# Optimization experiments

Measured on AMD Instinct MI355X. Metric: run time of the kernel, lower is better.

The kernel has to match this reference:

```python
import jax, jax.numpy as jnp
import numpy as np

N1, N2, D = 256, 256, 1024


def setup_inputs() -> dict:
    key = jax.random.key(0)
    k1, k2, k3, k4, k5, k6, k7 = jax.random.split(key, 7)
    return {
        "features1": jax.random.normal(k1, (N1, D), dtype=jnp.float32),
        "features2": jax.random.normal(k2, (N2, D), dtype=jnp.float32),
        "mask_cross": jax.random.randint(k3, (N1, N2), 0, 2, dtype=jnp.int32),
        "mask1": jax.random.randint(k4, (N1, N1), 0, 2, dtype=jnp.int32),
        "mask2": jax.random.randint(k5, (N2, N2), 0, 2, dtype=jnp.int32),
        "mask_sents1": jax.random.randint(k6, (N1,), 0, 2, dtype=jnp.int32).astype(bool),
        "mask_sents2": jax.random.randint(k7, (N2,), 0, 2, dtype=jnp.int32).astype(bool),
    }


def _compute_loss(sim, mask, sel):
    # sim: [R, C] similarities; mask: [R, C] in {0,1}; sel: [R] row selector in {0,1}.
    # Torch code masked-selects rows (mask_sents) and pos/neg entries per row, then
    # sums -logsigmoid(sim_pos - sim_neg) over all (pos, neg) pairs. Rows with zero
    # pos or zero neg contribute 0 loss and 0 pairs, so the data-dependent branch is
    # exactly reproduced by multiplicative masking.
    mp = mask * sel[:, None]          # selected positive mask [R, C]
    mn = 1.0 - mask                   # negative mask [R, C]
    # -logsigmoid(x) == softplus(-x)
    nls = jax.nn.softplus(-(sim[:, :, None] - sim[:, None, :]))  # [R, C, C]
    loss = jnp.einsum('ij,ik,ijk->', mp, mn, nls)
    pair_num = jnp.sum(mp.sum(axis=1) * mn.sum(axis=1) * sel)
    return loss, pair_num


def reference(features1, features2, mask_cross, mask1, mask2, mask_sents1, mask_sents2):
    # sim_type == 'dot': no normalization; temperature is unused by the math.
    mc = mask_cross.astype(jnp.float32)
    m1 = mask1.astype(jnp.float32)
    m2 = mask2.astype(jnp.float32)
    s1 = mask_sents1.astype(jnp.float32)
    s2 = mask_sents2.astype(jnp.float32)

    sim12 = features1 @ features2.T   # [N1, N2]
    sim11 = features1 @ features1.T   # [N1, N1]
    sim22 = features2 @ features2.T   # [N2, N2]

    l1, p1 = _compute_loss(sim12, mc, s1)
    l2, p2 = _compute_loss(sim12.T, mc.T, s2)
    l3, p3 = _compute_loss(sim11, m1, s1)
    l4, p4 = _compute_loss(sim22, m2, s2)

    loss = l1 + l2 + l3 + l4
    pair_num = p1 + p2 + p3 + p4
    return jnp.where(pair_num > 0, loss / jnp.maximum(pair_num, 1.0), loss)
```

## Files before the change

### kernel.cpp

```cpp
#include <hip/hip_runtime.h>
#include <hip/hip_bf16.h>
#include <math.h>


#define NN 256
#define DD 1024

typedef __attribute__((ext_vector_type(8))) short short8;
typedef __attribute__((ext_vector_type(4))) float f32x4;

__device__ __forceinline__ unsigned short f32_to_bf16_rne(float x) {
    unsigned int u = __float_as_uint(x);
    u += 0x7fffu + ((u >> 16) & 1u);
    return (unsigned short)(u >> 16);
}

__global__ __launch_bounds__(256) void convert_prep_kernel(
        const float* __restrict__ f1, const float* __restrict__ f2,
        unsigned short* __restrict__ b1, unsigned short* __restrict__ b2,
        const void* ms1, const void* ms2,
        float* sel1, float* sel2,
        double* lossAcc, unsigned long long* pairAcc) {
    const int bid = blockIdx.x;
    const int tid = threadIdx.x;
    if (bid < 512) {
        const float* src = (bid < 256) ? f1 : f2;
        unsigned short* dst = (bid < 256) ? b1 : b2;
        int base = ((bid & 255) * 256 + tid) * 4;
        float4 v = *(const float4*)(src + base);
        ushort4 o;
        o.x = f32_to_bf16_rne(v.x);
        o.y = f32_to_bf16_rne(v.y);
        o.z = f32_to_bf16_rne(v.z);
        o.w = f32_to_bf16_rne(v.w);
        *(ushort4*)(dst + base) = o;
    } else {
        __shared__ int nz1, nz2;
        if (tid == 0) { nz1 = 0; nz2 = 0; }
        __syncthreads();
        const unsigned char* c1 = (const unsigned char*)ms1;
        const unsigned char* c2 = (const unsigned char*)ms2;
        if ((tid & 3) != 0) {
            if (c1[tid] != 0) atomicOr(&nz1, 1);
            if (c2[tid] != 0) atomicOr(&nz2, 1);
        }
        __syncthreads();
        sel1[tid] = (nz1 != 0) ? (c1[tid] ? 1.0f : 0.0f)
                               : (float)((const int*)ms1)[tid];
        sel2[tid] = (nz2 != 0) ? (c2[tid] ? 1.0f : 0.0f)
                               : (float)((const int*)ms2)[tid];
        if (tid == 0) { *lossAcc = 0.0; *pairAcc = 0ULL; }
    }
}

__global__ __launch_bounds__(256) void gemm_mfma(
        const unsigned short* __restrict__ b1,
        const unsigned short* __restrict__ b2,
        float* __restrict__ sims) {
    const int gwave = blockIdx.x * 4 + (threadIdx.x >> 6);
    const int m = gwave >> 8;
    const int t = gwave & 255;
    const int tr = t >> 4, tc = t & 15;
    const unsigned short* A  = (m == 2) ? b2 : b1;
    const unsigned short* Bm = (m == 0) ? b2 : ((m == 1) ? b1 : b2);
    float* C = sims + m * (NN * NN);

    const int lane = threadIdx.x & 63;
    const int r = lane & 15;
    const int quad = lane >> 4;

    const unsigned short* aptr = A  + (tr * 16 + r) * DD + quad * 8;
    const unsigned short* bptr = Bm + (tc * 16 + r) * DD + quad * 8;

    f32x4 acc = {0.f, 0.f, 0.f, 0.f};
#pragma unroll 8
    for (int k0 = 0; k0 < DD; k0 += 32) {
        short8 af = *(const short8*)(aptr + k0);
        short8 bf = *(const short8*)(bptr + k0);
        acc = __builtin_amdgcn_mfma_f32_16x16x32_bf16(af, bf, acc, 0, 0, 0);
    }
    const int row0 = tr * 16 + quad * 4;
    const int col = tc * 16 + (lane & 15);
#pragma unroll
    for (int rr = 0; rr < 4; rr++) {
        C[(row0 + rr) * NN + col] = acc[rr];
    }
}

__global__ __launch_bounds__(256) void loss_kernel(
        const float* __restrict__ sims,
        const int* __restrict__ mc,
        const int* __restrict__ m1,
        const int* __restrict__ m2,
        const float* __restrict__ sel1,
        const float* __restrict__ sel2,
        double* lossAcc, unsigned long long* pairAcc) {
    const int i = blockIdx.x;
    const int c = blockIdx.y;
    const int tid = threadIdx.x;

    const float* sim12 = sims;
    const float* sim11 = sims + NN * NN;
    const float* sim22 = sims + 2 * NN * NN;

    float sel, simv;
    int maskv;
    if (c == 0) {
        sel = sel1[i]; simv = sim12[i * NN + tid]; maskv = mc[i * NN + tid];
    } else if (c == 1) {
        sel = sel2[i]; simv = sim12[tid * NN + i]; maskv = mc[tid * NN + i];
    } else if (c == 2) {
        sel = sel1[i]; simv = sim11[i * NN + tid]; maskv = m1[i * NN + tid];
    } else {
        sel = sel2[i]; simv = sim22[i * NN + tid]; maskv = m2[i * NN + tid];
    }
    if (sel == 0.0f) return;

    const float LOG2E = 1.4426950408889634f;
    const float LN2   = 0.6931471805599453f;

    __shared__ float sPos[NN];
    __shared__ float sNeg[NN];
    __shared__ int wcnt[4];
    __shared__ float red[4];

    const int lane = tid & 63;
    const int w = tid >> 6;
    const bool pos = (maskv != 0);
    unsigned long long bal = __ballot(pos);
    if (lane == 0) wcnt[w] = __popcll(bal);
    __syncthreads();

    int posBase = 0, np_ = 0;
#pragma unroll
    for (int q = 0; q < 4; q++) {
        int v = wcnt[q];
        if (q < w) posBase += v;
        np_ += v;
    }
    const int nn_ = NN - np_;

    const unsigned long long ltmask = (1ull << lane) - 1ull;
    const int pp = __popcll(bal & ltmask);
    const float tval = simv * LOG2E;
    if (pos) sPos[posBase + pp] = tval;
    else     sNeg[(w * 64 - posBase) + (lane - pp)] = tval;
    __syncthreads();

    if (np_ == 0 || nn_ == 0) return;
    if (tid == 0) atomicAdd(pairAcc, (unsigned long long)(np_ * nn_));

    const float tn = (tid < nn_) ? sNeg[tid] : -1e30f;
    float accL = 0.f, accM = 0.f;
    for (int jj = 0; jj < np_; jj++) {
        float sp = sPos[jj];
        float x2 = tn - sp;
        float e = __builtin_amdgcn_exp2f(-fabsf(x2));
        accL += __builtin_amdgcn_logf(1.0f + e);
        accM += fmaxf(x2, 0.0f);
    }
    float local = (accL + accM) * LN2;

#pragma unroll
    for (int off = 32; off > 0; off >>= 1) local += __shfl_down(local, off, 64);
    if (lane == 0) red[w] = local;
    __syncthreads();
    if (tid == 0) {
        double bsum = (double)red[0] + (double)red[1] +
                      (double)red[2] + (double)red[3];
        atomicAdd(lossAcc, bsum);
    }
}

__global__ void finalize_kernel(const double* lossAcc,
                                const unsigned long long* pairAcc,
                                float* out) {
    double loss = *lossAcc;
    unsigned long long p = *pairAcc;
    double r = (p > 0ULL) ? (loss / (double)p) : loss;
    out[0] = (float)r;
}

extern "C" void kernel_launch(void* const* d_in, const int* in_sizes, int n_in,
                              void* d_out, int out_size, void* d_ws, size_t ws_size,
                              hipStream_t stream) {
    const float* f1 = (const float*)d_in[0];
    const float* f2 = (const float*)d_in[1];
    const int* mc = (const int*)d_in[2];
    const int* m1 = (const int*)d_in[3];
    const int* m2 = (const int*)d_in[4];
    const void* ms1 = d_in[5];
    const void* ms2 = d_in[6];

    char* ws = (char*)d_ws;
    float* sims          = (float*)ws;
    unsigned short* b1   = (unsigned short*)(ws + 786432);
    unsigned short* b2   = (unsigned short*)(ws + 1310720);
    float* sel1          = (float*)(ws + 1835008);
    float* sel2          = (float*)(ws + 1836032);
    double* lossAcc      = (double*)(ws + 1837056);
    unsigned long long* pairAcc = (unsigned long long*)(ws + 1837064);

    convert_prep_kernel<<<513, 256, 0, stream>>>(f1, f2, b1, b2, ms1, ms2,
                                                 sel1, sel2, lossAcc, pairAcc);
    gemm_mfma<<<192, 256, 0, stream>>>(b1, b2, sims);
    loss_kernel<<<dim3(256, 4), 256, 0, stream>>>(sims, mc, m1, m2, sel1, sel2,
                                                  lossAcc, pairAcc);
    finalize_kernel<<<1, 1, 0, stream>>>(lossAcc, pairAcc, (float*)d_out);
}
```

Baseline: 90.29 us.

## Fuse bf16 conversion into GEMM and finalize into loss kernel via done counter

The GEMM now reads fp32 features directly and converts them to bf16 in registers, so the separate conversion pass and its intermediate buffers are gone. The finalize step moves into the loss kernel through a last-block-done atomic counter. Together these take the pipeline from four launches to two. The cost is that the GEMM fetches twice as many bytes per MFMA and does redundant conversions, and every loss block does an extra atomic and fence.

```diff
diff --git a/kernel.cpp b/kernel.cpp
--- a/kernel.cpp
+++ b/kernel.cpp
@@ -1,5 +1,4 @@
 #include <hip/hip_runtime.h>
-#include <hip/hip_bf16.h>
 #include <math.h>
 
 
@@ -15,26 +14,16 @@
     return (unsigned short)(u >> 16);
 }
 
-__global__ __launch_bounds__(256) void convert_prep_kernel(
+__global__ __launch_bounds__(256) void gemm_prep_kernel(
         const float* __restrict__ f1, const float* __restrict__ f2,
-        unsigned short* __restrict__ b1, unsigned short* __restrict__ b2,
         const void* ms1, const void* ms2,
+        float* __restrict__ sims,
         float* sel1, float* sel2,
-        double* lossAcc, unsigned long long* pairAcc) {
+        double* lossAcc, unsigned long long* pairAcc, unsigned int* doneCnt) {
     const int bid = blockIdx.x;
     const int tid = threadIdx.x;
-    if (bid < 512) {
-        const float* src = (bid < 256) ? f1 : f2;
-        unsigned short* dst = (bid < 256) ? b1 : b2;
-        int base = ((bid & 255) * 256 + tid) * 4;
-        float4 v = *(const float4*)(src + base);
-        ushort4 o;
-        o.x = f32_to_bf16_rne(v.x);
-        o.y = f32_to_bf16_rne(v.y);
-        o.z = f32_to_bf16_rne(v.z);
-        o.w = f32_to_bf16_rne(v.w);
-        *(ushort4*)(dst + base) = o;
-    } else {
+
+    if (bid == 192) {
         __shared__ int nz1, nz2;
         if (tid == 0) { nz1 = 0; nz2 = 0; }
         __syncthreads();
@@ -49,34 +38,49 @@
                                : (float)((const int*)ms1)[tid];
         sel2[tid] = (nz2 != 0) ? (c2[tid] ? 1.0f : 0.0f)
                                : (float)((const int*)ms2)[tid];
-        if (tid == 0) { *lossAcc = 0.0; *pairAcc = 0ULL; }
-    }
-}
-
-__global__ __launch_bounds__(256) void gemm_mfma(
-        const unsigned short* __restrict__ b1,
-        const unsigned short* __restrict__ b2,
-        float* __restrict__ sims) {
-    const int gwave = blockIdx.x * 4 + (threadIdx.x >> 6);
+        if (tid == 0) { *lossAcc = 0.0; *pairAcc = 0ULL; *doneCnt = 0u; }
+        return;
+    }
+
+    const int gwave = bid * 4 + (tid >> 6);
     const int m = gwave >> 8;
     const int t = gwave & 255;
     const int tr = t >> 4, tc = t & 15;
-    const unsigned short* A  = (m == 2) ? b2 : b1;
-    const unsigned short* Bm = (m == 0) ? b2 : ((m == 1) ? b1 : b2);
+    const float* A  = (m == 2) ? f2 : f1;
+    const float* Bm = (m == 0) ? f2 : ((m == 1) ? f1 : f2);
     float* C = sims + m * (NN * NN);
 
-    const int lane = threadIdx.x & 63;
+    const int lane = tid & 63;
     const int r = lane & 15;
     const int quad = lane >> 4;
 
-    const unsigned short* aptr = A  + (tr * 16 + r) * DD + quad * 8;
-    const unsigned short* bptr = Bm + (tc * 16 + r) * DD + quad * 8;
+    const float* aptr = A  + (tr * 16 + r) * DD + quad * 8;
+    const float* bptr = Bm + (tc * 16 + r) * DD + quad * 8;
 
     f32x4 acc = {0.f, 0.f, 0.f, 0.f};
-#pragma unroll 8
+#pragma unroll 4
     for (int k0 = 0; k0 < DD; k0 += 32) {
-        short8 af = *(const short8*)(aptr + k0);
-        short8 bf = *(const short8*)(bptr + k0);
+        float4 a0 = *(const float4*)(aptr + k0);
+        float4 a1 = *(const float4*)(aptr + k0 + 4);
+        float4 b0 = *(const float4*)(bptr + k0);
+        float4 b1 = *(const float4*)(bptr + k0 + 4);
+        short8 af, bf;
+        af[0] = (short)f32_to_bf16_rne(a0.x);
+        af[1] = (short)f32_to_bf16_rne(a0.y);
+        af[2] = (short)f32_to_bf16_rne(a0.z);
+        af[3] = (short)f32_to_bf16_rne(a0.w);
+        af[4] = (short)f32_to_bf16_rne(a1.x);
+        af[5] = (short)f32_to_bf16_rne(a1.y);
+        af[6] = (short)f32_to_bf16_rne(a1.z);
+        af[7] = (short)f32_to_bf16_rne(a1.w);
+        bf[0] = (short)f32_to_bf16_rne(b0.x);
+        bf[1] = (short)f32_to_bf16_rne(b0.y);
+        bf[2] = (short)f32_to_bf16_rne(b0.z);
+        bf[3] = (short)f32_to_bf16_rne(b0.w);
+        bf[4] = (short)f32_to_bf16_rne(b1.x);
+        bf[5] = (short)f32_to_bf16_rne(b1.y);
+        bf[6] = (short)f32_to_bf16_rne(b1.z);
+        bf[7] = (short)f32_to_bf16_rne(b1.w);
         acc = __builtin_amdgcn_mfma_f32_16x16x32_bf16(af, bf, acc, 0, 0, 0);
     }
     const int row0 = tr * 16 + quad * 4;
@@ -87,14 +91,15 @@
     }
 }
 
-__global__ __launch_bounds__(256) void loss_kernel(
+__global__ __launch_bounds__(256) void loss_finalize_kernel(
         const float* __restrict__ sims,
         const int* __restrict__ mc,
         const int* __restrict__ m1,
         const int* __restrict__ m2,
         const float* __restrict__ sel1,
         const float* __restrict__ sel2,
-        double* lossAcc, unsigned long long* pairAcc) {
+        double* lossAcc, unsigned long long* pairAcc,
+        unsigned int* doneCnt, float* out) {
     const int i = blockIdx.x;
     const int c = blockIdx.y;
     const int tid = threadIdx.x;
@@ -103,82 +108,93 @@
     const float* sim11 = sims + NN * NN;
     const float* sim22 = sims + 2 * NN * NN;
 
-    float sel, simv;
-    int maskv;
-    if (c == 0) {
-        sel = sel1[i]; simv = sim12[i * NN + tid]; maskv = mc[i * NN + tid];
-    } else if (c == 1) {
-        sel = sel2[i]; simv = sim12[tid * NN + i]; maskv = mc[tid * NN + i];
-    } else if (c == 2) {
-        sel = sel1[i]; simv = sim11[i * NN + tid]; maskv = m1[i * NN + tid];
-    } else {
-        sel = sel2[i]; simv = sim22[i * NN + tid]; maskv = m2[i * NN + tid];
-    }
-    if (sel == 0.0f) return;
-
-    const float LOG2E = 1.4426950408889634f;
-    const float LN2   = 0.6931471805599453f;
-
-    __shared__ float sPos[NN];
-    __shared__ float sNeg[NN];
-    __shared__ int wcnt[4];
-    __shared__ float red[4];
-
-    const int lane = tid & 63;
-    const int w = tid >> 6;
-    const bool pos = (maskv != 0);
-    unsigned long long bal = __ballot(pos);
-    if (lane == 0) wcnt[w] = __popcll(bal);
-    __syncthreads();
-
-    int posBase = 0, np_ = 0;
+    float sel;
+    if (c == 0)      sel = sel1[i];
+    else if (c == 1) sel = sel2[i];
+    else if (c == 2) sel = sel1[i];
+    else             sel = sel2[i];
+
+    if (sel != 0.0f) {
+        float simv;
+        int maskv;
+        if (c == 0) {
+            simv = sim12[i * NN + tid]; maskv = mc[i * NN + tid];
+        } else if (c == 1) {
+            simv = sim12[tid * NN + i]; maskv = mc[tid * NN + i];
+        } else if (c == 2) {
+            simv = sim11[i * NN + tid]; maskv = m1[i * NN + tid];
+        } else {
+            simv = sim22[i * NN + tid]; maskv = m2[i * NN + tid];
+        }
+
+        const float LOG2E = 1.4426950408889634f;
+        const float LN2   = 0.6931471805599453f;
+
+        __shared__ float sPos[NN];
+        __shared__ float sNeg[NN];
+        __shared__ int wcnt[4];
+        __shared__ float red[4];
+
+        const int lane = tid & 63;
+        const int w = tid >> 6;
+        const bool pos = (maskv != 0);
+        unsigned long long bal = __ballot(pos);
+        if (lane == 0) wcnt[w] = __popcll(bal);
+        __syncthreads();
+
+        int posBase = 0, np_ = 0;
 #pragma unroll
-    for (int q = 0; q < 4; q++) {
-        int v = wcnt[q];
-        if (q < w) posBase += v;
-        np_ += v;
-    }
-    const int nn_ = NN - np_;
-
-    const unsigned long long ltmask = (1ull << lane) - 1ull;
-    const int pp = __popcll(bal & ltmask);
-    const float tval = simv * LOG2E;
-    if (pos) sPos[posBase + pp] = tval;
-    else     sNeg[(w * 64 - posBase) + (lane - pp)] = tval;
-    __syncthreads();
-
-    if (np_ == 0 || nn_ == 0) return;
-    if (tid == 0) atomicAdd(pairAcc, (unsigned long long)(np_ * nn_));
-
-    const float tn = (tid < nn_) ? sNeg[tid] : -1e30f;
-    float accL = 0.f, accM = 0.f;
-    for (int jj = 0; jj < np_; jj++) {
-        float sp = sPos[jj];
-        float x2 = tn - sp;
-        float e = __builtin_amdgcn_exp2f(-fabsf(x2));
-        accL += __builtin_amdgcn_logf(1.0f + e);
-        accM += fmaxf(x2, 0.0f);
-    }
-    float local = (accL + accM) * LN2;
+        for (int q = 0; q < 4; q++) {
+            int v = wcnt[q];
+            if (q < w) posBase += v;
+            np_ += v;
+        }
+        const int nn_ = NN - np_;
+
+        const unsigned long long ltmask = (1ull << lane) - 1ull;
+        const int pp = __popcll(bal & ltmask);
+        const float tval = simv * LOG2E;
+        if (pos) sPos[posBase + pp] = tval;
+        else     sNeg[(w * 64 - posBase) + (lane - pp)] = tval;
+        __syncthreads();
+
+        if (np_ != 0 && nn_ != 0) {
+            if (tid == 0) atomicAdd(pairAcc, (unsigned long long)(np_ * nn_));
+
+            const float tn = (tid < nn_) ? sNeg[tid] : -1e30f;
+            float accL = 0.f, accM = 0.f;
+            for (int jj = 0; jj < np_; jj++) {
+                float sp = sPos[jj];
+                float x2 = tn - sp;
+                float e = __builtin_amdgcn_exp2f(-fabsf(x2));
+                accL += __builtin_amdgcn_logf(1.0f + e);
+                accM += fmaxf(x2, 0.0f);
+            }
+            float local = (accL + accM) * LN2;
 
 #pragma unroll
-    for (int off = 32; off > 0; off >>= 1) local += __shfl_down(local, off, 64);
-    if (lane == 0) red[w] = local;
-    __syncthreads();
+            for (int off = 32; off > 0; off >>= 1)
+                local += __shfl_down(local, off, 64);
+            if (lane == 0) red[w] = local;
+            __syncthreads();
+            if (tid == 0) {
+                double bsum = (double)red[0] + (double)red[1] +
+                              (double)red[2] + (double)red[3];
+                atomicAdd(lossAcc, bsum);
+            }
+        }
+    }
+
     if (tid == 0) {
-        double bsum = (double)red[0] + (double)red[1] +
-                      (double)red[2] + (double)red[3];
-        atomicAdd(lossAcc, bsum);
-    }
-}
-
-__global__ void finalize_kernel(const double* lossAcc,
-                                const unsigned long long* pairAcc,
-                                float* out) {
-    double loss = *lossAcc;
-    unsigned long long p = *pairAcc;
-    double r = (p > 0ULL) ? (loss / (double)p) : loss;
-    out[0] = (float)r;
+        __threadfence();
+        unsigned int old = atomicAdd(doneCnt, 1u);
+        if (old == 1023u) {
+            double loss = atomicAdd(lossAcc, 0.0);
+            unsigned long long p = atomicAdd(pairAcc, 0ULL);
+            double r = (p > 0ULL) ? (loss / (double)p) : loss;
+            out[0] = (float)r;
+        }
+    }
 }
 
 extern "C" void kernel_launch(void* const* d_in, const int* in_sizes, int n_in,
@@ -194,17 +210,16 @@
 
     char* ws = (char*)d_ws;
     float* sims          = (float*)ws;
-    unsigned short* b1   = (unsigned short*)(ws + 786432);
-    unsigned short* b2   = (unsigned short*)(ws + 1310720);
-    float* sel1          = (float*)(ws + 1835008);
-    float* sel2          = (float*)(ws + 1836032);
-    double* lossAcc      = (double*)(ws + 1837056);
-    unsigned long long* pairAcc = (unsigned long long*)(ws + 1837064);
-
-    convert_prep_kernel<<<513, 256, 0, stream>>>(f1, f2, b1, b2, ms1, ms2,
-                                                 sel1, sel2, lossAcc, pairAcc);
-    gemm_mfma<<<192, 256, 0, stream>>>(b1, b2, sims);
-    loss_kernel<<<dim3(256, 4), 256, 0, stream>>>(sims, mc, m1, m2, sel1, sel2,
-                                                  lossAcc, pairAcc);
-    finalize_kernel<<<1, 1, 0, stream>>>(lossAcc, pairAcc, (float*)d_out);
-}
+    float* sel1          = (float*)(ws + 786432);
+    float* sel2          = (float*)(ws + 787456);
+    double* lossAcc      = (double*)(ws + 788480);
+    unsigned long long* pairAcc = (unsigned long long*)(ws + 788488);
+    unsigned int* doneCnt = (unsigned int*)(ws + 788496);
+
+    gemm_prep_kernel<<<193, 256, 0, stream>>>(f1, f2, ms1, ms2, sims,
+                                              sel1, sel2, lossAcc, pairAcc,
+                                              doneCnt);
+    loss_finalize_kernel<<<dim3(256, 4), 256, 0, stream>>>(
+        sims, mc, m1, m2, sel1, sel2, lossAcc, pairAcc, doneCnt,
+        (float*)d_out);
+}
```

Measured after the change: 118.2 us. 31.0% more time.

## Fuse finalize into loss kernel via last-block counter; one wave per GEMM block

Applied to the files above, without the earlier changes.

Removes the separate single-thread finalize launch. Every loss block now bumps a done counter, and the last block computes the final ratio, which means early-returning blocks must still take part. The GEMM also moves from 192 blocks of 4 waves to 768 single-wave blocks, so its waves spread across more CUs. The cost is extra atomics per block and a dependence on atomic ordering when the last block reads the final totals.

```diff
diff --git a/kernel.cpp b/kernel.cpp
--- a/kernel.cpp
+++ b/kernel.cpp
@@ -1,5 +1,4 @@
 #include <hip/hip_runtime.h>
-#include <hip/hip_bf16.h>
 #include <math.h>
 
 
@@ -20,7 +19,7 @@
         unsigned short* __restrict__ b1, unsigned short* __restrict__ b2,
         const void* ms1, const void* ms2,
         float* sel1, float* sel2,
-        double* lossAcc, unsigned long long* pairAcc) {
+        double* lossAcc, unsigned long long* pairAcc, unsigned int* doneCnt) {
     const int bid = blockIdx.x;
     const int tid = threadIdx.x;
     if (bid < 512) {
@@ -49,15 +48,15 @@
                                : (float)((const int*)ms1)[tid];
         sel2[tid] = (nz2 != 0) ? (c2[tid] ? 1.0f : 0.0f)
                                : (float)((const int*)ms2)[tid];
-        if (tid == 0) { *lossAcc = 0.0; *pairAcc = 0ULL; }
-    }
-}
-
-__global__ __launch_bounds__(256) void gemm_mfma(
+        if (tid == 0) { *lossAcc = 0.0; *pairAcc = 0ULL; *doneCnt = 0u; }
+    }
+}
+
+__global__ __launch_bounds__(64) void gemm_mfma(
         const unsigned short* __restrict__ b1,
         const unsigned short* __restrict__ b2,
         float* __restrict__ sims) {
-    const int gwave = blockIdx.x * 4 + (threadIdx.x >> 6);
+    const int gwave = blockIdx.x;
     const int m = gwave >> 8;
     const int t = gwave & 255;
     const int tr = t >> 4, tc = t & 15;
@@ -87,14 +86,15 @@
     }
 }
 
-__global__ __launch_bounds__(256) void loss_kernel(
+__global__ __launch_bounds__(256) void loss_finalize_kernel(
         const float* __restrict__ sims,
         const int* __restrict__ mc,
         const int* __restrict__ m1,
         const int* __restrict__ m2,
         const float* __restrict__ sel1,
         const float* __restrict__ sel2,
-        double* lossAcc, unsigned long long* pairAcc) {
+        double* lossAcc, unsigned long long* pairAcc,
+        unsigned int* doneCnt, float* out) {
     const int i = blockIdx.x;
     const int c = blockIdx.y;
     const int tid = threadIdx.x;
@@ -103,82 +103,94 @@
     const float* sim11 = sims + NN * NN;
     const float* sim22 = sims + 2 * NN * NN;
 
-    float sel, simv;
-    int maskv;
-    if (c == 0) {
-        sel = sel1[i]; simv = sim12[i * NN + tid]; maskv = mc[i * NN + tid];
-    } else if (c == 1) {
-        sel = sel2[i]; simv = sim12[tid * NN + i]; maskv = mc[tid * NN + i];
-    } else if (c == 2) {
-        sel = sel1[i]; simv = sim11[i * NN + tid]; maskv = m1[i * NN + tid];
-    } else {
-        sel = sel2[i]; simv = sim22[i * NN + tid]; maskv = m2[i * NN + tid];
-    }
-    if (sel == 0.0f) return;
-
-    const float LOG2E = 1.4426950408889634f;
-    const float LN2   = 0.6931471805599453f;
-
-    __shared__ float sPos[NN];
-    __shared__ float sNeg[NN];
-    __shared__ int wcnt[4];
-    __shared__ float red[4];
-
-    const int lane = tid & 63;
-    const int w = tid >> 6;
-    const bool pos = (maskv != 0);
-    unsigned long long bal = __ballot(pos);
-    if (lane == 0) wcnt[w] = __popcll(bal);
-    __syncthreads();
-
-    int posBase = 0, np_ = 0;
+    const float sel = (c == 0 || c == 2) ? sel1[i] : sel2[i];
+
+    int np_ = 0, nn_ = 0;
+    double bsum = 0.0;
+
+    if (sel != 0.0f) {
+        float simv;
+        int maskv;
+        if (c == 0) {
+            simv = sim12[i * NN + tid]; maskv = mc[i * NN + tid];
+        } else if (c == 1) {
+            simv = sim12[tid * NN + i]; maskv = mc[tid * NN + i];
+        } else if (c == 2) {
+            simv = sim11[i * NN + tid]; maskv = m1[i * NN + tid];
+        } else {
+            simv = sim22[i * NN + tid]; maskv = m2[i * NN + tid];
+        }
+
+        const float LOG2E = 1.4426950408889634f;
+        const float LN2   = 0.6931471805599453f;
+
+        __shared__ float sPos[NN];
+        __shared__ float sNeg[NN];
+        __shared__ int wcnt[4];
+        __shared__ float red[4];
+
+        const int lane = tid & 63;
+        const int w = tid >> 6;
+        const bool pos = (maskv != 0);
+        unsigned long long bal = __ballot(pos);
+        if (lane == 0) wcnt[w] = __popcll(bal);
+        __syncthreads();
+
+        int posBase = 0;
 #pragma unroll
-    for (int q = 0; q < 4; q++) {
-        int v = wcnt[q];
-        if (q < w) posBase += v;
-        np_ += v;
-    }
-    const int nn_ = NN - np_;
-
-    const unsigned long long ltmask = (1ull << lane) - 1ull;
-    const int pp = __popcll(bal & ltmask);
-    const float tval = simv * LOG2E;
-    if (pos) sPos[posBase + pp] = tval;
-    else     sNeg[(w * 64 - posBase) + (lane - pp)] = tval;
-    __syncthreads();
-
-    if (np_ == 0 || nn_ == 0) return;
-    if (tid == 0) atomicAdd(pairAcc, (unsigned long long)(np_ * nn_));
-
-    const float tn = (tid < nn_) ? sNeg[tid] : -1e30f;
-    float accL = 0.f, accM = 0.f;
-    for (int jj = 0; jj < np_; jj++) {
-        float sp = sPos[jj];
-        float x2 = tn - sp;
-        float e = __builtin_amdgcn_exp2f(-fabsf(x2));
-        accL += __builtin_amdgcn_logf(1.0f + e);
-        accM += fmaxf(x2, 0.0f);
-    }
-    float local = (accL + accM) * LN2;
+        for (int q = 0; q < 4; q++) {
+            int v = wcnt[q];
+            if (q < w) posBase += v;
+            np_ += v;
+        }
+        nn_ = NN - np_;
+
+        const unsigned long long ltmask = (1ull << lane) - 1ull;
+        const int pp = __popcll(bal & ltmask);
+        const float tval = simv * LOG2E;
+        if (pos) sPos[posBase + pp] = tval;
+        else     sNeg[(w * 64 - posBase) + (lane - pp)] = tval;
+        __syncthreads();
+
+        if (np_ != 0 && nn_ != 0) {
+            const float tn = (tid < nn_) ? sNeg[tid] : -1e30f;
+            float accL = 0.f, accM = 0.f;
+            for (int jj = 0; jj < np_; jj++) {
+                float sp = sPos[jj];
+                float x2 = tn - sp;
+                float e = __builtin_amdgcn_exp2f(-fabsf(x2));
+                accL += __builtin_amdgcn_logf(1.0f + e);
+                accM += fmaxf(x2, 0.0f);
+            }
+            float local = (accL + accM) * LN2;
 
 #pragma unroll
-    for (int off = 32; off > 0; off >>= 1) local += __shfl_down(local, off, 64);
-    if (lane == 0) red[w] = local;
-    __syncthreads();
+            for (int off = 32; off > 0; off >>= 1)
+                local += __shfl_down(local, off, 64);
+            if (lane == 0) red[w] = local;
+            __syncthreads();
+            if (tid == 0) {
+                bsum = (double)red[0] + (double)red[1] +
+                       (double)red[2] + (double)red[3];
+            }
+        }
+    }
+
     if (tid == 0) {
-        double bsum = (double)red[0] + (double)red[1] +
-                      (double)red[2] + (double)red[3];
-        atomicAdd(lossAcc, bsum);
-    }
-}
-
-__global__ void finalize_kernel(const double* lossAcc,
-                                const unsigned long long* pairAcc,
-                                float* out) {
-    double loss = *lossAcc;
-    unsigned long long p = *pairAcc;
-    double r = (p > 0ULL) ? (loss / (double)p) : loss;
-    out[0] = (float)r;
+        if (np_ != 0 && nn_ != 0) {
+            unsigned long long pprev =
+                atomicAdd(pairAcc, (unsigned long long)(np_ * nn_));
+            double lprev = atomicAdd(lossAcc, bsum);
+            __asm__ volatile("" :: "v"(pprev), "v"(lprev));
+        }
+        unsigned int old = atomicAdd(doneCnt, 1u);
+        if (old == 1023u) {
+            double loss = atomicAdd(lossAcc, 0.0);
+            unsigned long long p = atomicAdd(pairAcc, 0ULL);
+            double r = (p > 0ULL) ? (loss / (double)p) : loss;
+            out[0] = (float)r;
+        }
+    }
 }
 
 extern "C" void kernel_launch(void* const* d_in, const int* in_sizes, int n_in,
@@ -200,11 +212,13 @@
     float* sel2          = (float*)(ws + 1836032);
     double* lossAcc      = (double*)(ws + 1837056);
     unsigned long long* pairAcc = (unsigned long long*)(ws + 1837064);
+    unsigned int* doneCnt = (unsigned int*)(ws + 1837072);
 
     convert_prep_kernel<<<513, 256, 0, stream>>>(f1, f2, b1, b2, ms1, ms2,
-                                                 sel1, sel2, lossAcc, pairAcc);
-    gemm_mfma<<<192, 256, 0, stream>>>(b1, b2, sims);
-    loss_kernel<<<dim3(256, 4), 256, 0, stream>>>(sims, mc, m1, m2, sel1, sel2,
-                                                  lossAcc, pairAcc);
-    finalize_kernel<<<1, 1, 0, stream>>>(lossAcc, pairAcc, (float*)d_out);
-}
+                                                 sel1, sel2, lossAcc, pairAcc,
+                                                 doneCnt);
+    gemm_mfma<<<768, 64, 0, stream>>>(b1, b2, sims);
+    loss_finalize_kernel<<<dim3(256, 4), 256, 0, stream>>>(
+        sims, mc, m1, m2, sel1, sel2, lossAcc, pairAcc, doneCnt,
+        (float*)d_out);
+}
```

Result: slower. 101.3 us (+12.2%).
